# Kernel tuning notes

Measured on AMD Instinct MI355X. Metric: run time of the kernel, lower is better.

The kernel has to match this reference:

```python
import jax, jax.numpy as jnp
import numpy as np

T = 16000        # signal length
N1 = 120         # first-order filters (J=12, Q=10)
NPSI2 = 14       # second-order filterbank size (Q2=1)
NPAIR = 553      # second-order coefficients -> 120 + 553 = 673 channels
SUB1 = 8         # subsample U1 before order 2
T2 = T // SUB1   # 2000
STR1 = 1000      # lowpass stride at length T  -> 16 output samples
STR2 = T2 // (T // STR1)  # 125 -> 16 output samples
LOG_EPS = 1e-6
BN_EPS = 1e-5


def _gauss_hat(N, xi, sigma):
    om = np.arange(N) / N
    return np.exp(-((om - xi) ** 2) / (2.0 * sigma ** 2)).astype(np.float32)


def _filterbank():
    Q = 10.0
    xi1 = 0.45 * 2.0 ** (-np.arange(N1) / Q)
    sig1 = np.maximum(xi1 * 0.1, 2.0 / T)
    psi1 = np.stack([_gauss_hat(T, x, s) for x, s in zip(xi1, sig1)])
    phi1 = _gauss_hat(T, 0.0, 0.4 / STR1)
    xi2 = 0.45 * 2.0 ** (-np.arange(NPSI2, dtype=np.float64))
    sig2 = np.maximum(xi2 * 0.2, 2.0 / T2)
    psi2 = np.stack([_gauss_hat(T2, x, s) for x, s in zip(xi2, sig2)])
    phi2 = _gauss_hat(T2, 0.0, 0.4 / STR2)
    pairs = [(i, j) for i in range(N1) for j in range(NPSI2) if xi2[j] < xi1[i] / 2.0]
    pairs = pairs[:NPAIR]
    assert len(pairs) == NPAIR
    pi1 = np.array([p[0] for p in pairs], np.int32)
    pi2 = np.array([p[1] for p in pairs], np.int32)
    return psi1, phi1, psi2, phi2, pi1, pi2


def setup_inputs():
    key = jax.random.key(0)
    ks = jax.random.split(key, 8)
    psi1, phi1, psi2, phi2, pi1, pi2 = _filterbank()
    B = 32
    inp = {
        "x": jax.random.normal(ks[0], (B, 1, T), jnp.float32),
        "psi1_hat": jnp.asarray(psi1),
        "phi1_hat": jnp.asarray(phi1),
        "psi2_hat": jnp.asarray(psi2),
        "phi2_hat": jnp.asarray(phi2),
        "gamma": jnp.ones((673,), jnp.float32),
        "beta": jnp.zeros((673,), jnp.float32),
        "W1": jax.random.normal(ks[1], (300, 673), jnp.float32) * 0.04,
        "b1": jnp.zeros((300,), jnp.float32),
        "W2": jax.random.normal(ks[2], (90, 300), jnp.float32) * 0.06,
        "b2": jnp.zeros((90,), jnp.float32),
        "W3": jax.random.normal(ks[3], (35, 90), jnp.float32) * 0.1,
        "b3": jnp.zeros((35,), jnp.float32),
        "pair_i1": jnp.asarray(pi1),
        "pair_i2": jnp.asarray(pi2),
    }
    return inp


def reference(x, psi1_hat, phi1_hat, psi2_hat, phi2_hat, gamma, beta,
              W1, b1, W2, b2, W3, b3, pair_i1, pair_i2):
    xs = x.squeeze(1)                                       # [B, T]
    Xf = jnp.fft.fft(xs)                                    # [B, T] c64
    # --- order 1: wavelet conv (freq-domain), modulus ---
    U1 = jnp.abs(jnp.fft.ifft(Xf[:, None, :] * psi1_hat[None]))        # [B, N1, T]
    # S1 = lowpass(U1) subsampled to 16 samples
    S1 = jnp.real(jnp.fft.ifft(jnp.fft.fft(U1) * phi1_hat))[..., ::STR1]  # [B, N1, 16]
    # --- order 2 on subsampled U1 ---
    U1sf = jnp.fft.fft(U1[..., ::SUB1])                     # [B, N1, T2]
    U2 = jnp.abs(jnp.fft.ifft(U1sf[:, pair_i1, :] * psi2_hat[pair_i2]))  # [B, NPAIR, T2]
    S2 = jnp.real(jnp.fft.ifft(jnp.fft.fft(U2) * phi2_hat))[..., ::STR2]  # [B, NPAIR, 16]
    S = jnp.concatenate([S1, S2], axis=1)                   # [B, 673, 16]
    # log-abs + temporal mean pooling
    f = jnp.mean(jnp.log(jnp.abs(S) + LOG_EPS), axis=-1)    # [B, 673]
    # BatchNorm1d (training mode: batch statistics)
    mu = jnp.mean(f, axis=0)
    var = jnp.var(f, axis=0)
    f = (f - mu) / jnp.sqrt(var + BN_EPS) * gamma + beta
    # MLP head
    h = jax.nn.relu(f @ W1.T + b1)
    h = jax.nn.relu(h @ W2.T + b2)
    return jax.nn.log_softmax(h @ W3.T + b3, axis=-1)
```

## Files before the change

### kernel.cpp

```cpp
#include <hip/hip_runtime.h>
#include <math.h>

typedef float2 cf;

__device__ __forceinline__ cf cadd(cf a, cf b){ return make_float2(a.x+b.x, a.y+b.y); }
__device__ __forceinline__ cf csub(cf a, cf b){ return make_float2(a.x-b.x, a.y-b.y); }
__device__ __forceinline__ cf cmul(cf a, cf b){ return make_float2(a.x*b.x - a.y*b.y, a.x*b.y + a.y*b.x); }

__device__ __forceinline__ int SW(int i){ return i ^ ((i>>4)&15); }
#define AT(x) s[SW(x)]
#define WFENCE asm volatile("" ::: "memory")

template<bool WAVE> __device__ __forceinline__ void SYf(){
  if constexpr (WAVE) { WFENCE; } else __syncthreads();
}

__device__ __forceinline__ int devB(int i){
  int jm = i/10 + 2;
  double kc = 900.0*exp2((double)(-jm));
  double sg = fmax(180.0*exp2((double)(-jm)), 2.0);
  return min(2000, (int)ceil(kc + 6.5*sg) + 1);
}

template<int N, int L, bool INV>
__device__ __forceinline__ void stage_r2(cf* __restrict__ s, const cf* __restrict__ tw, int tid, int nt){
  constexpr int Ls = L/2, nbf = N/2, tws = 16000/L;
  for (int q = tid; q < nbf; q += nt){
    int blk = q / Ls, j = q - blk*Ls;
    int base = blk*L + j;
    cf w1 = tw[tws*j]; if (INV) w1.y = -w1.y;
    if (!INV){
      cf a = AT(base), b = AT(base+Ls);
      AT(base) = cadd(a,b);
      AT(base+Ls) = cmul(csub(a,b), w1);
    } else {
      cf a = AT(base), b = cmul(AT(base+Ls), w1);
      AT(base) = cadd(a,b);
      AT(base+Ls) = csub(a,b);
    }
  }
}

template<int N, int L, bool INV>
__device__ __forceinline__ void stage_r4(cf* __restrict__ s, const cf* __restrict__ tw, int tid, int nt){
  constexpr int Ls = L/4, nbf = N/4, tws = 16000/L;
  for (int q = tid; q < nbf; q += nt){
    int blk = q / Ls, j = q - blk*Ls;
    int base = blk*L + j;
    cf w1 = tw[tws*j]; if (INV) w1.y = -w1.y;
    cf w2 = cmul(w1,w1), w3 = cmul(w2,w1);
    if (!INV){
      cf y0=AT(base), y1=AT(base+Ls), y2=AT(base+2*Ls), y3=AT(base+3*Ls);
      cf t0=cadd(y0,y2), t1=csub(y0,y2), t2=cadd(y1,y3), t3=csub(y1,y3);
      AT(base)      = cadd(t0,t2);
      AT(base+Ls)   = cmul(make_float2(t1.x + t3.y, t1.y - t3.x), w1);
      AT(base+2*Ls) = cmul(csub(t0,t2), w2);
      AT(base+3*Ls) = cmul(make_float2(t1.x - t3.y, t1.y + t3.x), w3);
    } else {
      cf z0=AT(base);
      cf z1=cmul(AT(base+Ls),   w1);
      cf z2=cmul(AT(base+2*Ls), w2);
      cf z3=cmul(AT(base+3*Ls), w3);
      cf t0=cadd(z0,z2), t1=csub(z0,z2), t2=cadd(z1,z3), t3=csub(z1,z3);
      AT(base)      = cadd(t0,t2);
      AT(base+Ls)   = make_float2(t1.x - t3.y, t1.y + t3.x);
      AT(base+2*Ls) = csub(t0,t2);
      AT(base+3*Ls) = make_float2(t1.x + t3.y, t1.y - t3.x);
    }
  }
}

template<int N, int L, bool INV>
__device__ __forceinline__ void stage_r5(cf* __restrict__ s, const cf* __restrict__ tw, int tid, int nt){
  constexpr int Ls = L/5, nbf = N/5, tws = 16000/L;
  const float C1 = 0.30901699437494742f, S1c = 0.95105651629515357f;
  const float C2 = -0.80901699437494745f, S2c = 0.58778525229247314f;
  for (int q = tid; q < nbf; q += nt){
    int blk = q / Ls, j = q - blk*Ls;
    int base = blk*L + j;
    cf w1 = tw[tws*j]; if (INV) w1.y = -w1.y;
    cf w2 = cmul(w1,w1), w3 = cmul(w2,w1), w4 = cmul(w2,w2);
    if (!INV){
      cf y0=AT(base), y1=AT(base+Ls), y2=AT(base+2*Ls), y3=AT(base+3*Ls), y4=AT(base+4*Ls);
      cf t1=cadd(y1,y4), t2=csub(y1,y4), t3=cadd(y2,y3), t4=csub(y2,y3);
      cf z0 = cadd(y0, cadd(t1,t3));
      cf m1 = make_float2(y0.x + C1*t1.x + C2*t3.x, y0.y + C1*t1.y + C2*t3.y);
      cf m2 = make_float2(y0.x + C2*t1.x + C1*t3.x, y0.y + C2*t1.y + C1*t3.y);
      cf wa = make_float2(S1c*t2.x + S2c*t4.x, S1c*t2.y + S2c*t4.y);
      cf wb = make_float2(S2c*t2.x - S1c*t4.x, S2c*t2.y - S1c*t4.y);
      cf o1 = make_float2(m1.x + wa.y, m1.y - wa.x);
      cf o4 = make_float2(m1.x - wa.y, m1.y + wa.x);
      cf o2 = make_float2(m2.x + wb.y, m2.y - wb.x);
      cf o3 = make_float2(m2.x - wb.y, m2.y + wb.x);
      AT(base) = z0;
      AT(base+Ls)   = cmul(o1,w1);
      AT(base+2*Ls) = cmul(o2,w2);
      AT(base+3*Ls) = cmul(o3,w3);
      AT(base+4*Ls) = cmul(o4,w4);
    } else {
      cf z0=AT(base);
      cf z1=cmul(AT(base+Ls),   w1);
      cf z2=cmul(AT(base+2*Ls), w2);
      cf z3=cmul(AT(base+3*Ls), w3);
      cf z4=cmul(AT(base+4*Ls), w4);
      cf t1=cadd(z1,z4), t2=csub(z1,z4), t3=cadd(z2,z3), t4=csub(z2,z3);
      cf y0 = cadd(z0, cadd(t1,t3));
      cf m1 = make_float2(z0.x + C1*t1.x + C2*t3.x, z0.y + C1*t1.y + C2*t3.y);
      cf m2 = make_float2(z0.x + C2*t1.x + C1*t3.x, z0.y + C2*t1.y + C1*t3.y);
      cf wa = make_float2(S1c*t2.x + S2c*t4.x, S1c*t2.y + S2c*t4.y);
      cf wb = make_float2(S2c*t2.x - S1c*t4.x, S2c*t2.y - S1c*t4.y);
      AT(base)      = y0;
      AT(base+Ls)   = make_float2(m1.x - wa.y, m1.y + wa.x);
      AT(base+2*Ls) = make_float2(m2.x - wb.y, m2.y + wb.x);
      AT(base+3*Ls) = make_float2(m2.x + wb.y, m2.y - wb.x);
      AT(base+4*Ls) = make_float2(m1.x + wa.y, m1.y - wa.x);
    }
  }
}

template<bool INV>
__device__ void fft16000(cf* s, const cf* tw, int tid, int nt){
  if (!INV){
    stage_r5<16000,16000,false>(s,tw,tid,nt); __syncthreads();
    stage_r5<16000, 3200,false>(s,tw,tid,nt); __syncthreads();
    stage_r5<16000,  640,false>(s,tw,tid,nt); __syncthreads();
    stage_r4<16000,  128,false>(s,tw,tid,nt); __syncthreads();
    stage_r4<16000,   32,false>(s,tw,tid,nt); __syncthreads();
    stage_r4<16000,    8,false>(s,tw,tid,nt); __syncthreads();
    stage_r2<16000,    2,false>(s,tw,tid,nt); __syncthreads();
  } else {
    stage_r2<16000,    2,true >(s,tw,tid,nt); __syncthreads();
    stage_r4<16000,    8,true >(s,tw,tid,nt); __syncthreads();
    stage_r4<16000,   32,true >(s,tw,tid,nt); __syncthreads();
    stage_r4<16000,  128,true >(s,tw,tid,nt); __syncthreads();
    stage_r5<16000,  640,true >(s,tw,tid,nt); __syncthreads();
    stage_r5<16000, 3200,true >(s,tw,tid,nt); __syncthreads();
    stage_r5<16000,16000,true >(s,tw,tid,nt); __syncthreads();
  }
}

template<bool INV>
__device__ void fft2000(cf* s, const cf* tw, int tid, int nt){
  if (!INV){
    stage_r5<2000,2000,false>(s,tw,tid,nt); __syncthreads();
    stage_r5<2000, 400,false>(s,tw,tid,nt); __syncthreads();
    stage_r5<2000,  80,false>(s,tw,tid,nt); __syncthreads();
    stage_r4<2000,  16,false>(s,tw,tid,nt); __syncthreads();
    stage_r4<2000,   4,false>(s,tw,tid,nt); __syncthreads();
  } else {
    stage_r4<2000,   4,true >(s,tw,tid,nt); __syncthreads();
    stage_r4<2000,  16,true >(s,tw,tid,nt); __syncthreads();
    stage_r5<2000,  80,true >(s,tw,tid,nt); __syncthreads();
    stage_r5<2000, 400,true >(s,tw,tid,nt); __syncthreads();
    stage_r5<2000,2000,true >(s,tw,tid,nt); __syncthreads();
  }
}

__device__ void fft8000i(cf* s, const cf* tw, int tid, int nt){
  stage_r4<8000,   4,true>(s,tw,tid,nt); __syncthreads();
  stage_r4<8000,  16,true>(s,tw,tid,nt); __syncthreads();
  stage_r4<8000,  64,true>(s,tw,tid,nt); __syncthreads();
  stage_r5<8000, 320,true>(s,tw,tid,nt); __syncthreads();
  stage_r5<8000,1600,true>(s,tw,tid,nt); __syncthreads();
  stage_r5<8000,8000,true>(s,tw,tid,nt); __syncthreads();
}
__device__ void fft4000i(cf* s, const cf* tw, int tid, int nt){
  stage_r2<4000,   2,true>(s,tw,tid,nt); __syncthreads();
  stage_r4<4000,   8,true>(s,tw,tid,nt); __syncthreads();
  stage_r4<4000,  32,true>(s,tw,tid,nt); __syncthreads();
  stage_r5<4000, 160,true>(s,tw,tid,nt); __syncthreads();
  stage_r5<4000, 800,true>(s,tw,tid,nt); __syncthreads();
  stage_r5<4000,4000,true>(s,tw,tid,nt); __syncthreads();
}
__device__ void fft1000i(cf* s, const cf* tw, int tid, int nt){
  stage_r2<1000,   2,true>(s,tw,tid,nt); __syncthreads();
  stage_r4<1000,   8,true>(s,tw,tid,nt); __syncthreads();
  stage_r5<1000,  40,true>(s,tw,tid,nt); __syncthreads();
  stage_r5<1000, 200,true>(s,tw,tid,nt); __syncthreads();
  stage_r5<1000,1000,true>(s,tw,tid,nt); __syncthreads();
}
__device__ void fft500i(cf* s, const cf* tw, int tid, int nt){
  stage_r4<500,  4,true>(s,tw,tid,nt); __syncthreads();
  stage_r5<500, 20,true>(s,tw,tid,nt); __syncthreads();
  stage_r5<500,100,true>(s,tw,tid,nt); __syncthreads();
  stage_r5<500,500,true>(s,tw,tid,nt); __syncthreads();
}
__device__ __forceinline__ void fft250w(cf* s, const cf* tw, int lane){
  stage_r2<250,  2,true>(s,tw,lane,64); WFENCE;
  stage_r5<250, 10,true>(s,tw,lane,64); WFENCE;
  stage_r5<250, 50,true>(s,tw,lane,64); WFENCE;
  stage_r5<250,250,true>(s,tw,lane,64); WFENCE;
}

template<int M, bool INV, bool WAVE>
__device__ __forceinline__ void fftg(cf* s, const cf* tw, int tid, int nt){
  if constexpr (M==2000){
    if constexpr (INV){
      stage_r4<2000,4,true>(s,tw,tid,nt); SYf<WAVE>();
      stage_r4<2000,16,true>(s,tw,tid,nt); SYf<WAVE>();
      stage_r5<2000,80,true>(s,tw,tid,nt); SYf<WAVE>();
      stage_r5<2000,400,true>(s,tw,tid,nt); SYf<WAVE>();
      stage_r5<2000,2000,true>(s,tw,tid,nt); SYf<WAVE>();
    } else {
      stage_r5<2000,2000,false>(s,tw,tid,nt); SYf<WAVE>();
      stage_r5<2000,400,false>(s,tw,tid,nt); SYf<WAVE>();
      stage_r5<2000,80,false>(s,tw,tid,nt); SYf<WAVE>();
      stage_r4<2000,16,false>(s,tw,tid,nt); SYf<WAVE>();
      stage_r4<2000,4,false>(s,tw,tid,nt); SYf<WAVE>();
    }
  } else if constexpr (M==1600){
    if constexpr (INV){
      stage_r4<1600,4,true>(s,tw,tid,nt); SYf<WAVE>();
      stage_r4<1600,16,true>(s,tw,tid,nt); SYf<WAVE>();
      stage_r4<1600,64,true>(s,tw,tid,nt); SYf<WAVE>();
      stage_r5<1600,320,true>(s,tw,tid,nt); SYf<WAVE>();
      stage_r5<1600,1600,true>(s,tw,tid,nt); SYf<WAVE>();
    } else {
      stage_r5<1600,1600,false>(s,tw,tid,nt); SYf<WAVE>();
      stage_r5<1600,320,false>(s,tw,tid,nt); SYf<WAVE>();
      stage_r4<1600,64,false>(s,tw,tid,nt); SYf<WAVE>();
      stage_r4<1600,16,false>(s,tw,tid,nt); SYf<WAVE>();
      stage_r4<1600,4,false>(s,tw,tid,nt); SYf<WAVE>();
    }
  } else if constexpr (M==640){
    if constexpr (INV){
      stage_r2<640,2,true>(s,tw,tid,nt); SYf<WAVE>();
      stage_r4<640,8,true>(s,tw,tid,nt); SYf<WAVE>();
      stage_r4<640,32,true>(s,tw,tid,nt); SYf<WAVE>();
      stage_r4<640,128,true>(s,tw,tid,nt); SYf<WAVE>();
      stage_r5<640,640,true>(s,tw,tid,nt); SYf<WAVE>();
    } else {
      stage_r5<640,640,false>(s,tw,tid,nt); SYf<WAVE>();
      stage_r4<640,128,false>(s,tw,tid,nt); SYf<WAVE>();
      stage_r4<640,32,false>(s,tw,tid,nt); SYf<WAVE>();
      stage_r4<640,8,false>(s,tw,tid,nt); SYf<WAVE>();
      stage_r2<640,2,false>(s,tw,tid,nt); SYf<WAVE>();
    }
  } else if constexpr (M==320){
    if constexpr (INV){
      stage_r4<320,4,true>(s,tw,tid,nt); SYf<WAVE>();
      stage_r4<320,16,true>(s,tw,tid,nt); SYf<WAVE>();
      stage_r4<320,64,true>(s,tw,tid,nt); SYf<WAVE>();
      stage_r5<320,320,true>(s,tw,tid,nt); SYf<WAVE>();
    } else {
      stage_r5<320,320,false>(s,tw,tid,nt); SYf<WAVE>();
      stage_r4<320,64,false>(s,tw,tid,nt); SYf<WAVE>();
      stage_r4<320,16,false>(s,tw,tid,nt); SYf<WAVE>();
      stage_r4<320,4,false>(s,tw,tid,nt); SYf<WAVE>();
    }
  } else if constexpr (M==200){
    if constexpr (INV){
      stage_r2<200,2,true>(s,tw,tid,nt); SYf<WAVE>();
      stage_r4<200,8,true>(s,tw,tid,nt); SYf<WAVE>();
      stage_r5<200,40,true>(s,tw,tid,nt); SYf<WAVE>();
      stage_r5<200,200,true>(s,tw,tid,nt); SYf<WAVE>();
    } else {
      stage_r5<200,200,false>(s,tw,tid,nt); SYf<WAVE>();
      stage_r5<200,40,false>(s,tw,tid,nt); SYf<WAVE>();
      stage_r4<200,8,false>(s,tw,tid,nt); SYf<WAVE>();
      stage_r2<200,2,false>(s,tw,tid,nt); SYf<WAVE>();
    }
  } else {
    if constexpr (INV){
      stage_r2<160,2,true>(s,tw,tid,nt); SYf<WAVE>();
      stage_r4<160,8,true>(s,tw,tid,nt); SYf<WAVE>();
      stage_r4<160,32,true>(s,tw,tid,nt); SYf<WAVE>();
      stage_r5<160,160,true>(s,tw,tid,nt); SYf<WAVE>();
    } else {
      stage_r5<160,160,false>(s,tw,tid,nt); SYf<WAVE>();
      stage_r4<160,32,false>(s,tw,tid,nt); SYf<WAVE>();
      stage_r4<160,8,false>(s,tw,tid,nt); SYf<WAVE>();
      stage_r2<160,2,false>(s,tw,tid,nt); SYf<WAVE>();
    }
  }
}

__device__ __forceinline__ int pos16000(int k){
  int k0=k%5; k/=5; int k1=k%5; k/=5; int k2=k%5; k/=5;
  int k3=k&3; k>>=2; int k4=k&3; k>>=2; int k5=k&3; k>>=2;
  return k0*3200 + k1*640 + k2*128 + k3*32 + k4*8 + k5*2 + k;
}
__device__ __forceinline__ int pos8000(int k){
  int k0=k%5; k/=5; int k1=k%5; k/=5; int k2=k%5; k/=5;
  int k3=k&3, k4=(k>>2)&3, k5=k>>4;
  return k0*1600 + k1*320 + k2*64 + k3*16 + k4*4 + k5;
}
__device__ __forceinline__ int pos4000(int k){
  int k0=k%5; k/=5; int k1=k%5; k/=5; int k2=k%5; k/=5;
  int k3=k&3, k4=(k>>2)&3, k5=k>>4;
  return k0*800 + k1*160 + k2*32 + k3*8 + k4*2 + k5;
}
__device__ __forceinline__ int pos2000(int k){
  int k0=k%5; k/=5; int k1=k%5; k/=5; int k2=k%5; k/=5;
  int k3=k&3, k4=k>>2;
  return k0*400 + k1*80 + k2*16 + k3*4 + k4;
}
__device__ __forceinline__ int pos1600(int k){
  int k0=k%5; k/=5; int k1=k%5; k/=5;
  int k2=k&3; k>>=2; int k3=k&3; k>>=2;
  return k0*320 + k1*64 + k2*16 + k3*4 + k;
}
__device__ __forceinline__ int pos1000(int k){
  int k0=k%5; k/=5; int k1=k%5; k/=5; int k2=k%5; k/=5;
  int k3=k&3, k4=k>>2;
  return k0*200 + k1*40 + k2*8 + k3*2 + k4;
}
__device__ __forceinline__ int pos640(int k){
  int k0=k%5; k/=5;
  int k1=k&3; k>>=2; int k2=k&3; k>>=2; int k3=k&3; k>>=2;
  return k0*128 + k1*32 + k2*8 + k3*2 + k;
}
__device__ __forceinline__ int pos500(int k){
  int k0=k%5; k/=5; int k1=k%5; k/=5; int k2=k%5; k/=5;
  return k0*100 + k1*20 + k2*4 + k;
}
__device__ __forceinline__ int pos320(int k){
  int k0=k%5; k/=5;
  int k1=k&3; k>>=2; int k2=k&3; k>>=2;
  return k0*64 + k1*16 + k2*4 + k;
}
__device__ __forceinline__ int pos250(int k){
  int k0=k%5; k/=5; int k1=k%5; k/=5; int k2=k%5; k/=5;
  return k0*50 + k1*10 + k2*2 + k;
}
__device__ __forceinline__ int pos200(int k){
  int k0=k%5; k/=5; int k1=k%5; k/=5;
  int k2=k&3, k3=k>>2;
  return k0*40 + k1*8 + k2*2 + k3;
}
__device__ __forceinline__ int pos160(int k){
  int k0=k%5; k/=5;
  int k1=k&3; k>>=2; int k2=k&3; k>>=2;
  return k0*32 + k1*8 + k2*2 + k;
}

template<int M> __device__ __forceinline__ int posM(int k){
  if constexpr (M==16000) return pos16000(k);
  else if constexpr (M==8000) return pos8000(k);
  else if constexpr (M==4000) return pos4000(k);
  else return pos2000(k);
}
template<int M> __device__ __forceinline__ int posN(int k){
  if constexpr (M==2000) return pos2000(k);
  else if constexpr (M==1600) return pos1600(k);
  else if constexpr (M==640) return pos640(k);
  else if constexpr (M==320) return pos320(k);
  else if constexpr (M==200) return pos200(k);
  else return pos160(k);
}
template<int M> __device__ __forceinline__ void fftM_inv(cf* s, const cf* tw, int tid, int nt){
  if constexpr (M==16000) fft16000<true>(s,tw,tid,nt);
  else if constexpr (M==8000) fft8000i(s,tw,tid,nt);
  else if constexpr (M==4000) fft4000i(s,tw,tid,nt);
  else fft2000<true>(s,tw,tid,nt);
}


__global__ void k_tw(cf* __restrict__ tw){
  int j = blockIdx.x*blockDim.x + threadIdx.x;
  if (j < 16000){
    double a = -6.283185307179586476925286766559 * (double)j / 16000.0;
    tw[j] = make_float2((float)cos(a), (float)sin(a));
  }
}

__global__ void k_btab(const float* __restrict__ phi1, const float* __restrict__ phi2,
                       float* __restrict__ h1g, float* __restrict__ h2g){
  int i = blockIdx.x*blockDim.x + threadIdx.x;
  const double TWO_PI = 6.283185307179586476925286766559;
  if (i < 5201){
    int d = i - 2600;
    double a = 0.0;
    for (int k = 0; k < 64; ++k) a += (double)phi1[k]*cos(TWO_PI*(double)(k*d)/16000.0);
    h1g[i] = (float)(a/16000.0 - (double)phi1[0]/32000.0);
  } else if (i == 5201){
    h1g[5201] = phi1[0]*(1.f/32000.f);
  } else if (i < 5202 + 661){
    int j = i - 5202; int d = j - 330;
    double a = 0.0;
    for (int k = 0; k < 64; ++k) a += (double)phi2[k]*cos(TWO_PI*(double)(k*d)/2000.0);
    h2g[j] = (float)(a/2000.0 - (double)phi2[0]/4000.0);
  } else if (i == 5202 + 661){
    h2g[661] = phi2[0]*(1.f/4000.f);
  }
}

__global__ __launch_bounds__(1024) void k_classify(const int* __restrict__ pi2,
                                                   int* __restrict__ list5, int* __restrict__ list4){
  __shared__ int w5[16], w4[16];
  int p = threadIdx.x;
  for (int t = p; t < 493; t += 1024) list5[t] = 0;
  for (int t = p; t < 60;  t += 1024) list4[t] = 0;
  bool valid = p < 553;
  int j2 = valid ? pi2[p] : 99;
  bool f5 = valid && (j2 >= 5);
  bool f4 = valid && (j2 < 5);
  unsigned long long m5 = __ballot(f5);
  unsigned long long m4 = __ballot(f4);
  int lane = p & 63, wid = p >> 6;
  if (lane == 0){ w5[wid] = __popcll(m5); w4[wid] = __popcll(m4); }
  __syncthreads();
  if (valid){
    int b5 = 0, b4 = 0;
    for (int w = 0; w < wid; ++w){ b5 += w5[w]; b4 += w4[w]; }
    unsigned long long lm = (1ull << lane) - 1ull;
    if (f5) list5[b5 + __popcll(m5 & lm)] = p;
    if (f4) list4[b4 + __popcll(m4 & lm)] = p;
  }
}

__global__ __launch_bounds__(1024) void k_fftx(const float* __restrict__ x, cf* __restrict__ Xf,
                                               const cf* __restrict__ tw){
  extern __shared__ cf s[];
  int b = blockIdx.x;
  int tid = threadIdx.x, nt = blockDim.x;
  for (int n = tid; n < 16000; n += nt) AT(n) = make_float2(x[b*16000 + n], 0.f);
  __syncthreads();
  fft16000<false>(s, tw, tid, nt);
  for (int k = tid; k < 16000; k += nt) Xf[b*16000 + k] = AT(pos16000(k));
}

template<int M, int ST, int NF, int I0, int NT>
__global__ __launch_bounds__(NT) void kf(const cf* __restrict__ Xf, const float* __restrict__ psi1,
                                         const float* __restrict__ h1g, const cf* __restrict__ tw,
                                         cf* __restrict__ U1sf, float* __restrict__ S1){
  extern __shared__ cf s[];
  constexpr int NW = NT/64;
  int b = blockIdx.x / NF;
  int i = I0 + (blockIdx.x - b*NF);
  int tid = threadIdx.x, wid = tid>>6, lane = tid&63;
  double x1 = 0.45 * exp2((double)(-i) / 10.0);
  double kc = 16000.0 * x1;
  double sg = fmax(1600.0 * x1, 2.0);
  int k0 = max(0, (int)floor(kc - 6.5*sg));
  int k1 = min(16000, (int)ceil(kc + 6.5*sg) + 1);
  int W = k1 - k0;
  for (int n = tid; n < M; n += NT) s[n] = make_float2(0.f, 0.f);
  __syncthreads();
  const cf* X = Xf + (size_t)b*16000 + k0;
  const float* P = psi1 + (size_t)i*16000 + k0;
  for (int j = tid; j < W; j += NT){
    cf v = X[j]; float pf = P[j];
    int pp = posM<M>(j);
    AT(pp) = make_float2(v.x*pf, v.y*pf);
  }
  __syncthreads();
  fftM_inv<M>(s, tw, tid, NT);
  constexpr int R = (M + NT - 1)/NT;
  float mreg[R]; float tsum = 0.f;
  const float inv = 1.f/16000.f;
  #pragma unroll
  for (int r = 0; r < R; ++r){
    int n = tid + r*NT;
    if (n < M){ cf v = AT(n); mreg[r] = sqrtf(v.x*v.x + v.y*v.y)*inv; tsum += mreg[r]; }
    else mreg[r] = 0.f;
  }
  float* fl = (float*)s;
  float* part = (float*)(s + M);
  __syncthreads();
  #pragma unroll
  for (int r = 0; r < R; ++r){ int n = tid + r*NT; if (n < M) fl[n] = mreg[r]; }
  #pragma unroll
  for (int o = 32; o > 0; o >>= 1) tsum += __shfl_xor(tsum, o);
  if (lane == 0) part[wid] = tsum;
  __syncthreads();
  if (tid == 0){ float tt = 0.f; for (int w = 0; w < NW; ++w) tt += part[w]; part[NW] = tt; }
  __syncthreads();
  float stot = part[NW];
  float c1 = h1g[5201];
  for (int t = wid; t < 16; t += NW){
    int mlo = (1000*t - 2600)/ST;
    int mhi = (1000*t + 2600)/ST;
    float acc = 0.f;
    for (int m = mlo + lane; m <= mhi; m += 64){
      int mm = m; if (mm < 0) mm += M; else if (mm >= M) mm -= M;
      acc = fmaf(fl[mm], h1g[1000*t - m*ST + 2600], acc);
    }
    #pragma unroll
    for (int o = 32; o > 0; o >>= 1) acc += __shfl_xor(acc, o);
    if (lane == 0) S1[((size_t)b*120 + i)*16 + t] = (float)ST*(acc + c1*stot);
  }
  constexpr int K = 8/ST;
  float d0 = fl[tid*K];
  float d1 = 0.f;
  { int m2 = tid + 1024; if (m2 < 2000) d1 = fl[m2*K]; }
  __syncthreads();
  AT(tid) = make_float2(d0, 0.f);
  { int m2 = tid + 1024; if (m2 < 2000) AT(m2) = make_float2(d1, 0.f); }
  __syncthreads();
  fft2000<false>(s, tw, tid, NT);
  int B = devB(i);
  cf* out = U1sf + ((size_t)b*120 + i)*2000;
  for (int k = tid; k < B; k += NT) out[k] = AT(pos2000(k));
}

template<int M, int NF, int I0>
__global__ __launch_bounds__(256) void k_n2(const cf* __restrict__ Xf, const float* __restrict__ psi1,
                                            const float* __restrict__ phi1, const cf* __restrict__ tw,
                                            cf* __restrict__ U1sf, float* __restrict__ S1){
  extern __shared__ cf s[];
  int b = blockIdx.x / NF;
  int i = I0 + (blockIdx.x - b*NF);
  int tid = threadIdx.x, wid = tid>>6, lane = tid&63;
  double x1 = 0.45 * exp2((double)(-i)/10.0);
  double kc = 16000.0*x1, sg = fmax(1600.0*x1, 2.0);
  int k0 = max(0,(int)floor(kc-6.5*sg));
  int k1 = min(16000,(int)ceil(kc+6.5*sg)+1);
  int W = k1-k0;
  for (int n = tid; n < M; n += 256) s[n] = make_float2(0.f,0.f);
  __syncthreads();
  const cf* X = Xf + (size_t)b*16000 + k0;
  const float* P = psi1 + (size_t)i*16000 + k0;
  for (int j = tid; j < W; j += 256){
    cf v = X[j]; float pf = P[j];
    AT(posN<M>(j)) = make_float2(v.x*pf, v.y*pf);
  }
  __syncthreads();
  fftg<M,true,false>(s,tw,tid,256);
  for (int n = tid; n < M; n += 256){
    cf v = AT(n);
    AT(n) = make_float2(sqrtf(v.x*v.x+v.y*v.y)*(1.f/16000.f), 0.f);
  }
  __syncthreads();
  fftg<M,false,false>(s,tw,tid,256);
  {
    int k = lane;
    cf g = AT(posN<M>(k));
    float ph = phi1[k];
    float gx = g.x*ph, gy = g.y*ph;
    float* S1o = S1 + ((size_t)b*120+i)*16;
    for (int r = 0; r < 4; ++r){
      int t = wid + 4*r;
      cf e = tw[1000*((k*t)&15)];
      float val = gx*e.x + gy*e.y;
      #pragma unroll
      for (int o = 32; o > 0; o >>= 1) val += __shfl_xor(val, o);
      if (lane == 0) S1o[t] = val*(1.f/(float)M);
    }
  }
  int B = devB(i);
  const float sc = 2000.f/(float)M;
  cf* out = U1sf + ((size_t)b*120+i)*2000;
  for (int k = tid; k < B; k += 256){
    cf v = AT(posN<M>(k));
    out[k] = make_float2(v.x*sc, v.y*sc);
  }
}

template<int M, int SPAD, int NF, int I0, int WPB>
__global__ __launch_bounds__(WPB*64) void k_nw2(const cf* __restrict__ Xf, const float* __restrict__ psi1,
                                                const float* __restrict__ phi1, const cf* __restrict__ tw,
                                                cf* __restrict__ U1sf, float* __restrict__ S1){
  extern __shared__ cf sh[];
  int wid = threadIdx.x >> 6, lane = threadIdx.x & 63;
  int q = blockIdx.x*WPB + wid;
  int filt = q >> 5, b = q & 31;
  int i = I0 + filt;
  cf* s = sh + wid*SPAD;
  double x1 = 0.45 * exp2((double)(-i)/10.0);
  double kc = 16000.0*x1, sg = fmax(1600.0*x1, 2.0);
  int k0 = max(0,(int)floor(kc-6.5*sg));
  int k1 = min(16000,(int)ceil(kc+6.5*sg)+1);
  int W = k1-k0;
  for (int n = lane; n < SPAD; n += 64) s[n] = make_float2(0.f,0.f);
  WFENCE;
  const cf* X = Xf + (size_t)b*16000 + k0;
  const float* P = psi1 + (size_t)i*16000 + k0;
  for (int j = lane; j < W; j += 64){
    cf v = X[j]; float pf = P[j];
    AT(posN<M>(j)) = make_float2(v.x*pf, v.y*pf);
  }
  WFENCE;
  fftg<M,true,true>(s,tw,lane,64);
  for (int n = lane; n < M; n += 64){
    cf v = AT(n);
    AT(n) = make_float2(sqrtf(v.x*v.x+v.y*v.y)*(1.f/16000.f), 0.f);
  }
  WFENCE;
  fftg<M,false,true>(s,tw,lane,64);
  {
    int k = lane;
    cf g = AT(posN<M>(k));
    float ph = phi1[k];
    float gx = g.x*ph, gy = g.y*ph;
    float* S1o = S1 + ((size_t)b*120+i)*16;
    for (int t = 0; t < 16; ++t){
      cf e = tw[1000*((k*t)&15)];
      float val = gx*e.x + gy*e.y;
      #pragma unroll
      for (int o = 32; o > 0; o >>= 1) val += __shfl_xor(val, o);
      if (lane == 0) S1o[t] = val*(1.f/(float)M);
    }
  }
  int B = devB(i);
  const float sc = 2000.f/(float)M;
  cf* out = U1sf + ((size_t)b*120+i)*2000;
  for (int k = lane; k < B; k += 64){
    cf v = AT(posN<M>(k));
    out[k] = make_float2(v.x*sc, v.y*sc);
  }
}

__global__ __launch_bounds__(256) void k_sec5(const cf* __restrict__ U1sf, const float* __restrict__ psi2,
                                              const float* __restrict__ h2g, const cf* __restrict__ tw,
                                              const int* __restrict__ pi1, const int* __restrict__ pi2,
                                              const int* __restrict__ list5, float* __restrict__ S2){
  __shared__ cf sall[4*256];
  __shared__ float flall[4*256];
  int wid = threadIdx.x >> 6, lane = threadIdx.x & 63;
  int q = blockIdx.x*4 + wid;
  int p = list5[q >> 5];
  int b = q & 31;
  int i1 = pi1[p], j2 = pi2[p];
  cf* s = sall + wid*256;
  float* fl2 = flall + wid*256;
  double xc = exp2((double)(-j2));
  double kc = 900.0*xc, sg = fmax(180.0*xc, 2.0);
  int k0 = max(0, (int)floor(kc - 6.5*sg));
  int k1 = min(2000, (int)ceil(kc + 6.5*sg) + 1);
  int W = k1 - k0;
  for (int n = lane; n < 256; n += 64) s[n] = make_float2(0.f, 0.f);
  WFENCE;
  const cf* U = U1sf + (size_t)(b*120 + i1)*2000 + k0;
  const float* F = psi2 + j2*2000 + k0;
  for (int j = lane; j < W; j += 64){
    cf v = U[j]; float f = F[j];
    AT(pos250(j)) = make_float2(v.x*f, v.y*f);
  }
  WFENCE;
  fft250w(s, tw, lane);
  float tsum = 0.f;
  #pragma unroll
  for (int r = 0; r < 4; ++r){
    int n = lane + r*64;
    if (n < 250){
      cf v = AT(n);
      float mg = sqrtf(v.x*v.x + v.y*v.y)*(1.f/2000.f);
      fl2[n] = mg; tsum += mg;
    }
  }
  WFENCE;
  #pragma unroll
  for (int o = 32; o > 0; o >>= 1) tsum += __shfl_xor(tsum, o);
  float stot = tsum;
  float c2 = h2g[661];
  float* S2o = S2 + (size_t)(b*553 + p)*16;
  for (int t = 0; t < 16; ++t){
    int mlo = (125*t - 330 + 7) >> 3;
    int mhi = (125*t + 330) >> 3;
    float acc = 0.f;
    for (int m = mlo + lane; m <= mhi; m += 64){
      int mm = m; if (mm < 0) mm += 250; else if (mm >= 250) mm -= 250;
      acc = fmaf(fl2[mm], h2g[125*t - m*8 + 330], acc);
    }
    #pragma unroll
    for (int o = 32; o > 0; o >>= 1) acc += __shfl_xor(acc, o);
    if (lane == 0) S2o[t] = 8.f*(acc + c2*stot);
  }
}

__global__ __launch_bounds__(128) void k_secbig(const cf* __restrict__ U1sf, const float* __restrict__ psi2,
                                                const float* __restrict__ h2g, const cf* __restrict__ tw,
                                                const int* __restrict__ pi1, const int* __restrict__ pi2,
                                                const int* __restrict__ list4, float* __restrict__ S2){
  extern __shared__ cf s[];
  float* fl2 = (float*)(s + 2000);
  float* part = fl2 + 2000;
  int p = list4[blockIdx.x >> 5];
  int b = blockIdx.x & 31;
  int tid = threadIdx.x, wid = tid>>6, lane = tid&63;
  int i1 = pi1[p], j2 = pi2[p];
  int M2, s2l;
  if (j2 == 4){ M2 = 500;  s2l = 2; }
  else if (j2 == 3){ M2 = 1000; s2l = 1; }
  else { M2 = 2000; s2l = 0; }
  int ST2 = 1 << s2l;
  double xc = exp2((double)(-j2));
  double kc = 900.0*xc, sg = fmax(180.0*xc, 2.0);
  int k0 = max(0, (int)floor(kc - 6.5*sg));
  int k1 = min(2000, (int)ceil(kc + 6.5*sg) + 1);
  int W = k1 - k0;
  int M2r = (M2 + 15) & ~15;
  for (int n = tid; n < M2r; n += 128) s[n] = make_float2(0.f, 0.f);
  __syncthreads();
  const cf* U = U1sf + (size_t)(b*120 + i1)*2000 + k0;
  const float* F = psi2 + j2*2000 + k0;
  for (int j = tid; j < W; j += 128){
    cf v = U[j]; float f = F[j];
    int pp;
    if (M2 == 500) pp = pos500(j);
    else if (M2 == 1000) pp = pos1000(j);
    else pp = pos2000(j);
    AT(pp) = make_float2(v.x*f, v.y*f);
  }
  __syncthreads();
  if (M2 == 500) fft500i(s, tw, tid, 128);
  else if (M2 == 1000) fft1000i(s, tw, tid, 128);
  else fft2000<true>(s, tw, tid, 128);
  float tsum = 0.f;
  for (int n = tid; n < M2; n += 128){
    cf v = AT(n);
    float mg = sqrtf(v.x*v.x + v.y*v.y)*(1.f/2000.f);
    fl2[n] = mg; tsum += mg;
  }
  #pragma unroll
  for (int o = 32; o > 0; o >>= 1) tsum += __shfl_xor(tsum, o);
  if (lane == 0) part[wid] = tsum;
  __syncthreads();
  float stot = part[0] + part[1];
  float c2 = h2g[661];
  float* S2o = S2 + (size_t)(b*553 + p)*16;
  for (int r = 0; r < 8; ++r){
    int t = wid + (r<<1);
    int mlo = (125*t - 330 + ST2 - 1) >> s2l;
    int mhi = (125*t + 330) >> s2l;
    float acc = 0.f;
    for (int m = mlo + lane; m <= mhi; m += 64){
      int mm = m; if (mm < 0) mm += M2; else if (mm >= M2) mm -= M2;
      acc = fmaf(fl2[mm], h2g[125*t - m*ST2 + 330], acc);
    }
    #pragma unroll
    for (int o = 32; o > 0; o >>= 1) acc += __shfl_xor(acc, o);
    if (lane == 0) S2o[t] = (float)ST2*(acc + c2*stot);
  }
}

__global__ __launch_bounds__(64) void k_fbn(const float* __restrict__ S1, const float* __restrict__ S2,
                                            const float* __restrict__ g, const float* __restrict__ be,
                                            float* __restrict__ fn){
  int j = blockIdx.x;
  int b = threadIdx.x;
  float f = 0.f;
  if (b < 32){
    const float* src = (j < 120) ? (S1 + (b*120 + j)*16) : (S2 + (b*553 + (j-120))*16);
    float acc = 0.f;
    #pragma unroll
    for (int t = 0; t < 16; ++t) acc += logf(fabsf(src[t]) + 1e-6f);
    f = acc * (1.f/16.f);
  }
  float mu = f;
  #pragma unroll
  for (int o = 16; o > 0; o >>= 1) mu += __shfl_xor(mu, o);
  mu *= (1.f/32.f);
  float d = f - mu;
  float v = d*d;
  #pragma unroll
  for (int o = 16; o > 0; o >>= 1) v += __shfl_xor(v, o);
  v *= (1.f/32.f);
  float is = g[j] / sqrtf(v + 1e-5f);
  if (b < 32) fn[b*673 + j] = d*is + be[j];
}

__global__ __launch_bounds__(512) void k_mlp1(const float* __restrict__ fn,
                                              const float* __restrict__ W1, const float* __restrict__ b1,
                                              float* __restrict__ h1o){
  int task = blockIdx.x*8 + (threadIdx.x >> 6);
  int lane = threadIdx.x & 63;
  if (task >= 32*300) return;
  int b = task / 300, r = task - b*300;
  const float* f = fn + b*673;
  const float* w = W1 + r*673;
  float acc = 0.f;
  for (int k = lane; k < 673; k += 64) acc = fmaf(f[k], w[k], acc);
  #pragma unroll
  for (int o = 32; o > 0; o >>= 1) acc += __shfl_down(acc, o);
  if (lane == 0) h1o[b*300 + r] = fmaxf(acc + b1[r], 0.f);
}

__global__ __launch_bounds__(512) void k_mlp2(const float* __restrict__ h1,
                                              const float* __restrict__ W2, const float* __restrict__ b2,
                                              float* __restrict__ h2o){
  int task = blockIdx.x*8 + (threadIdx.x >> 6);
  int lane = threadIdx.x & 63;
  if (task >= 32*90) return;
  int b = task / 90, r = task - b*90;
  const float* h = h1 + b*300;
  const float* w = W2 + r*300;
  float acc = 0.f;
  for (int k = lane; k < 300; k += 64) acc = fmaf(h[k], w[k], acc);
  #pragma unroll
  for (int o = 32; o > 0; o >>= 1) acc += __shfl_down(acc, o);
  if (lane == 0) h2o[b*90 + r] = fmaxf(acc + b2[r], 0.f);
}

__global__ __launch_bounds__(256) void k_mlp3(const float* __restrict__ h2,
                                              const float* __restrict__ W3, const float* __restrict__ b3,
                                              float* __restrict__ out){
  __shared__ float lg[35];
  int b = blockIdx.x;
  int tid = threadIdx.x, wid = tid >> 6, lane = tid & 63;
  for (int r = wid; r < 35; r += 4){
    float acc = 0.f;
    for (int k = lane; k < 90; k += 64) acc = fmaf(h2[b*90 + k], W3[r*90 + k], acc);
    #pragma unroll
    for (int o = 32; o > 0; o >>= 1) acc += __shfl_down(acc, o);
    if (lane == 0) lg[r] = acc + b3[r];
  }
  __syncthreads();
  if (tid < 64){
    float v = (tid < 35) ? lg[tid] : -1e30f;
    float mx = v;
    #pragma unroll
    for (int o = 32; o > 0; o >>= 1) mx = fmaxf(mx, __shfl_xor(mx, o));
    float e = (tid < 35) ? expf(v - mx) : 0.f;
    float se = e;
    #pragma unroll
    for (int o = 32; o > 0; o >>= 1) se += __shfl_xor(se, o);
    if (tid < 35) out[b*35 + tid] = v - mx - logf(se);
  }
}


extern "C" void kernel_launch(void* const* d_in, const int* in_sizes, int n_in,
                              void* d_out, int out_size, void* d_ws, size_t ws_size,
                              hipStream_t stream){
  const float* x     = (const float*)d_in[0];
  const float* psi1  = (const float*)d_in[1];
  const float* phi1  = (const float*)d_in[2];
  const float* psi2  = (const float*)d_in[3];
  const float* phi2  = (const float*)d_in[4];
  const float* gamma = (const float*)d_in[5];
  const float* beta  = (const float*)d_in[6];
  const float* W1    = (const float*)d_in[7];
  const float* b1    = (const float*)d_in[8];
  const float* W2    = (const float*)d_in[9];
  const float* b2    = (const float*)d_in[10];
  const float* W3    = (const float*)d_in[11];
  const float* b3    = (const float*)d_in[12];
  const int*   pi1   = (const int*)d_in[13];
  const int*   pi2   = (const int*)d_in[14];

  char* ws = (char*)d_ws;
  constexpr size_t o_tw = 0;
  constexpr size_t o_Xf = o_tw + (size_t)16000*sizeof(cf);
  constexpr size_t o_U  = o_Xf + (size_t)32*16000*sizeof(cf);
  constexpr size_t o_S1 = o_U  + (size_t)3840*2000*sizeof(cf);
  constexpr size_t o_S2 = o_S1 + (size_t)3840*16*sizeof(float);
  constexpr size_t o_l5 = o_S2 + (size_t)17696*16*sizeof(float);
  constexpr size_t o_l4 = o_l5 + (size_t)512*sizeof(int);
  constexpr size_t o_fn = o_l4 + (size_t)64*sizeof(int);
  constexpr size_t o_h1 = o_fn + (size_t)32*673*sizeof(float);
  constexpr size_t o_h2 = o_h1 + (size_t)5202*sizeof(float);
  constexpr size_t o_m1 = o_h2 + (size_t)662*sizeof(float);
  constexpr size_t o_m2 = o_m1 + (size_t)32*300*sizeof(float);

  cf*    tw    = (cf*)(ws + o_tw);
  cf*    Xf    = (cf*)(ws + o_Xf);
  cf*    U1sf  = (cf*)(ws + o_U);
  float* S1b   = (float*)(ws + o_S1);
  float* S2b   = (float*)(ws + o_S2);
  int*   list5 = (int*)(ws + o_l5);
  int*   list4 = (int*)(ws + o_l4);
  float* fnbuf = (float*)(ws + o_fn);
  float* h1g   = (float*)(ws + o_h1);
  float* h2g   = (float*)(ws + o_h2);
  float* m1buf = (float*)(ws + o_m1);
  float* m2buf = (float*)(ws + o_m2);

  hipFuncSetAttribute((const void*)k_fftx, hipFuncAttributeMaxDynamicSharedMemorySize, 131072);
  hipFuncSetAttribute((const void*)kf<16000,1,13, 0,1024>, hipFuncAttributeMaxDynamicSharedMemorySize, 131072);
  hipFuncSetAttribute((const void*)kf< 8000,2,10,13,1024>, hipFuncAttributeMaxDynamicSharedMemorySize, 131072);

  k_tw<<<63, 256, 0, stream>>>(tw);
  k_btab<<<23, 256, 0, stream>>>(phi1, phi2, h1g, h2g);
  k_classify<<<1, 1024, 0, stream>>>(pi2, list5, list4);
  k_fftx<<<32, 1024, 128000, stream>>>(x, Xf, tw);
  kf<16000,1,13, 0,1024><<<32*13, 1024, 16000*8 + 17*4, stream>>>(Xf, psi1, h1g, tw, U1sf, S1b);
  kf< 8000,2,10,13,1024><<<32*10, 1024,  8000*8 + 17*4, stream>>>(Xf, psi1, h1g, tw, U1sf, S1b);
  kf< 4000,4,10,23,1024><<<32*10, 1024,  4000*8 + 17*4, stream>>>(Xf, psi1, h1g, tw, U1sf, S1b);
  k_n2<2000,10,33><<<32*10, 256, 2000*8, stream>>>(Xf, psi1, phi1, tw, U1sf, S1b);
  k_n2<1600,10,43><<<32*10, 256, 1600*8, stream>>>(Xf, psi1, phi1, tw, U1sf, S1b);
  k_nw2<640,640,10,53,4><<< 80, 256, 4*640*8, stream>>>(Xf, psi1, phi1, tw, U1sf, S1b);
  k_nw2<320,320,10,63,8><<< 40, 512, 8*320*8, stream>>>(Xf, psi1, phi1, tw, U1sf, S1b);
  k_nw2<200,208,10,73,8><<< 40, 512, 8*208*8, stream>>>(Xf, psi1, phi1, tw, U1sf, S1b);
  k_nw2<160,160,37,83,8><<<148, 512, 8*160*8, stream>>>(Xf, psi1, phi1, tw, U1sf, S1b);
  k_sec5<<<(493*32)/4, 256, 0, stream>>>(U1sf, psi2, h2g, tw, pi1, pi2, list5, S2b);
  k_secbig<<<60*32, 128, 2000*8 + 2000*4 + 4*4, stream>>>(U1sf, psi2, h2g, tw, pi1, pi2, list4, S2b);
  k_fbn<<<673, 64, 0, stream>>>(S1b, S2b, gamma, beta, fnbuf);
  k_mlp1<<<1200, 512, 0, stream>>>(fnbuf, W1, b1, m1buf);
  k_mlp2<<<360, 512, 0, stream>>>(m1buf, W2, b2, m2buf);
  k_mlp3<<<32, 256, 0, stream>>>(m2buf, W3, b3, (float*)d_out);
}
```

Baseline: 366.6 us.

## Split 16000-point inverse FFT into even/odd 8000-point halves per block

Replaces the 16000-point inverse FFT for the first 13 filters with two kernels, each computing an 8000-point inverse FFT of folded spectra (even and odd output samples via decimation in time). Each block then needs half the shared memory (64KB instead of 128KB), which allows two blocks per CU and more parallelism. The odd-phase kernel accumulates its lowpass contribution into S1, and only the even half produces the subsampled order-2 spectrum. The cost is an extra launch, a twiddle multiply, and a read-modify-write on S1 that depends on the two launches running in order on the stream.

```diff
diff --git a/kernel.cpp b/kernel.cpp
--- a/kernel.cpp
+++ b/kernel.cpp
@@ -172,18 +172,18 @@
   stage_r5<4000, 800,true>(s,tw,tid,nt); __syncthreads();
   stage_r5<4000,4000,true>(s,tw,tid,nt); __syncthreads();
 }
+__device__ void fft500i(cf* s, const cf* tw, int tid, int nt){
+  stage_r4<500,  4,true>(s,tw,tid,nt); __syncthreads();
+  stage_r5<500, 20,true>(s,tw,tid,nt); __syncthreads();
+  stage_r5<500,100,true>(s,tw,tid,nt); __syncthreads();
+  stage_r5<500,500,true>(s,tw,tid,nt); __syncthreads();
+}
 __device__ void fft1000i(cf* s, const cf* tw, int tid, int nt){
   stage_r2<1000,   2,true>(s,tw,tid,nt); __syncthreads();
   stage_r4<1000,   8,true>(s,tw,tid,nt); __syncthreads();
   stage_r5<1000,  40,true>(s,tw,tid,nt); __syncthreads();
   stage_r5<1000, 200,true>(s,tw,tid,nt); __syncthreads();
   stage_r5<1000,1000,true>(s,tw,tid,nt); __syncthreads();
-}
-__device__ void fft500i(cf* s, const cf* tw, int tid, int nt){
-  stage_r4<500,  4,true>(s,tw,tid,nt); __syncthreads();
-  stage_r5<500, 20,true>(s,tw,tid,nt); __syncthreads();
-  stage_r5<500,100,true>(s,tw,tid,nt); __syncthreads();
-  stage_r5<500,500,true>(s,tw,tid,nt); __syncthreads();
 }
 __device__ __forceinline__ void fft250w(cf* s, const cf* tw, int lane){
   stage_r2<250,  2,true>(s,tw,lane,64); WFENCE;
@@ -335,8 +335,7 @@
 }
 
 template<int M> __device__ __forceinline__ int posM(int k){
-  if constexpr (M==16000) return pos16000(k);
-  else if constexpr (M==8000) return pos8000(k);
+  if constexpr (M==8000) return pos8000(k);
   else if constexpr (M==4000) return pos4000(k);
   else return pos2000(k);
 }
@@ -349,8 +348,7 @@
   else return pos160(k);
 }
 template<int M> __device__ __forceinline__ void fftM_inv(cf* s, const cf* tw, int tid, int nt){
-  if constexpr (M==16000) fft16000<true>(s,tw,tid,nt);
-  else if constexpr (M==8000) fft8000i(s,tw,tid,nt);
+  if constexpr (M==8000) fft8000i(s,tw,tid,nt);
   else if constexpr (M==4000) fft4000i(s,tw,tid,nt);
   else fft2000<true>(s,tw,tid,nt);
 }
@@ -418,6 +416,90 @@
   __syncthreads();
   fft16000<false>(s, tw, tid, nt);
   for (int k = tid; k < 16000; k += nt) Xf[b*16000 + k] = AT(pos16000(k));
+}
+
+template<int PR, int NF, int I0>
+__global__ __launch_bounds__(1024) void kf16(const cf* __restrict__ Xf, const float* __restrict__ psi1,
+                                             const float* __restrict__ h1g, const cf* __restrict__ tw,
+                                             cf* __restrict__ U1sf, float* __restrict__ S1){
+  extern __shared__ cf s[];
+  float* part = (float*)(s + 8000);
+  int b = blockIdx.x / NF;
+  int i = I0 + (blockIdx.x - b*NF);
+  int tid = threadIdx.x, wid = tid>>6, lane = tid&63;
+  double x1 = 0.45 * exp2((double)(-i)/10.0);
+  double kc = 16000.0*x1, sg = fmax(1600.0*x1, 2.0);
+  int k0 = max(0,(int)floor(kc-6.5*sg));
+  int k1 = min(16000,(int)ceil(kc+6.5*sg)+1);
+  const cf* X = Xf + (size_t)b*16000;
+  const float* P = psi1 + (size_t)i*16000;
+  for (int j = tid; j < 8000; j += 1024){
+    cf acc = make_float2(0.f,0.f);
+    if (j >= k0 && j < k1){ cf v = X[j]; float pf = P[j]; acc.x = v.x*pf; acc.y = v.y*pf; }
+    int j2 = j + 8000;
+    if (j2 >= k0 && j2 < k1){
+      cf v = X[j2]; float pf = P[j2];
+      if (PR==0){ acc.x += v.x*pf; acc.y += v.y*pf; } else { acc.x -= v.x*pf; acc.y -= v.y*pf; }
+    }
+    if (PR==1){ cf ph = tw[j]; ph.y = -ph.y; acc = cmul(acc, ph); }
+    AT(pos8000(j)) = acc;
+  }
+  __syncthreads();
+  fft8000i(s, tw, tid, 1024);
+  float mreg[8]; float tsum = 0.f;
+  #pragma unroll
+  for (int r = 0; r < 8; ++r){
+    int n = tid + (r<<10);
+    cf v = AT(n);
+    mreg[r] = sqrtf(v.x*v.x+v.y*v.y)*(1.f/16000.f);
+    tsum += mreg[r];
+  }
+  float* fl = (float*)s;
+  __syncthreads();
+  #pragma unroll
+  for (int r = 0; r < 8; ++r) fl[tid + (r<<10)] = mreg[r];
+  #pragma unroll
+  for (int o = 32; o > 0; o >>= 1) tsum += __shfl_xor(tsum, o);
+  if (lane == 0) part[wid] = tsum;
+  __syncthreads();
+  if (tid == 0){ float tt = 0.f; for (int w = 0; w < 16; ++w) tt += part[w]; part[16] = tt; }
+  __syncthreads();
+  float stot = part[16];
+  float c1 = h1g[5201];
+  {
+    int t = wid;
+    float acc = 0.f;
+    if (PR == 0){
+      for (int u = -1300 + lane; u <= 1300; u += 64){
+        int m = 500*t - u;
+        if (m < 0) m += 8000; else if (m >= 8000) m -= 8000;
+        acc = fmaf(fl[m], h1g[2*u + 2600], acc);
+      }
+    } else {
+      for (int u = -1300 + lane; u <= 1299; u += 64){
+        int m = 500*t - u - 1;
+        if (m < 0) m += 8000; else if (m >= 8000) m -= 8000;
+        acc = fmaf(fl[m], h1g[2*u + 2601], acc);
+      }
+    }
+    #pragma unroll
+    for (int o = 32; o > 0; o >>= 1) acc += __shfl_xor(acc, o);
+    if (lane == 0){
+      float val = acc + c1*stot;
+      size_t idx = ((size_t)b*120 + i)*16 + t;
+      if (PR == 0) S1[idx] = val; else S1[idx] += val;
+    }
+  }
+  if constexpr (PR == 0){
+    cf* s2 = s + 4000;
+    __syncthreads();
+    for (int q = tid; q < 2000; q += 1024) s2[SW(q)] = make_float2(fl[4*q], 0.f);
+    __syncthreads();
+    fft2000<false>(s2, tw, tid, 1024);
+    int B = devB(i);
+    cf* out = U1sf + ((size_t)b*120 + i)*2000;
+    for (int k = tid; k < B; k += 1024) out[k] = s2[SW(pos2000(k))];
+  }
 }
 
 template<int M, int ST, int NF, int I0, int NT>
@@ -858,14 +940,13 @@
   float* m2buf = (float*)(ws + o_m2);
 
   hipFuncSetAttribute((const void*)k_fftx, hipFuncAttributeMaxDynamicSharedMemorySize, 131072);
-  hipFuncSetAttribute((const void*)kf<16000,1,13, 0,1024>, hipFuncAttributeMaxDynamicSharedMemorySize, 131072);
-  hipFuncSetAttribute((const void*)kf< 8000,2,10,13,1024>, hipFuncAttributeMaxDynamicSharedMemorySize, 131072);
 
   k_tw<<<63, 256, 0, stream>>>(tw);
   k_btab<<<23, 256, 0, stream>>>(phi1, phi2, h1g, h2g);
   k_classify<<<1, 1024, 0, stream>>>(pi2, list5, list4);
   k_fftx<<<32, 1024, 128000, stream>>>(x, Xf, tw);
-  kf<16000,1,13, 0,1024><<<32*13, 1024, 16000*8 + 17*4, stream>>>(Xf, psi1, h1g, tw, U1sf, S1b);
+  kf16<0,13,0><<<32*13, 1024, 8000*8 + 17*4, stream>>>(Xf, psi1, h1g, tw, U1sf, S1b);
+  kf16<1,13,0><<<32*13, 1024, 8000*8 + 17*4, stream>>>(Xf, psi1, h1g, tw, U1sf, S1b);
   kf< 8000,2,10,13,1024><<<32*10, 1024,  8000*8 + 17*4, stream>>>(Xf, psi1, h1g, tw, U1sf, S1b);
   kf< 4000,4,10,23,1024><<<32*10, 1024,  4000*8 + 17*4, stream>>>(Xf, psi1, h1g, tw, U1sf, S1b);
   k_n2<2000,10,33><<<32*10, 256, 2000*8, stream>>>(Xf, psi1, phi1, tw, U1sf, S1b);
```

Result: slower. 394.5 us (+7.6%).
